# Kernel tuning notes

Measured on AMD Instinct MI355X. Metric: run time of the kernel, lower is better.

The kernel has to match this reference:

```python
import jax, jax.numpy as jnp
import numpy as np

N = 4096  # matrix is [N, N]; all entries are nonzero 'edges' (uniform(0,1) fill)


def setup_inputs() -> dict:
    key = jax.random.key(0)
    k1, k2, k3 = jax.random.split(key, 3)
    matrix = jax.random.uniform(k1, (N, N), dtype=jnp.float32)
    drop_param = jax.random.normal(k2, (1,), dtype=jnp.float32)
    gamma = jax.random.normal(k3, (1,), dtype=jnp.float32)
    return {"matrix": matrix, "drop_param": drop_param, "gamma": gamma,
            "drop_ratio_pct": 20}


def reference(matrix, drop_param, gamma, drop_ratio_pct):
    # Flatten: every nonzero entry is an edge. With uniform fill all N*N entries
    # are edges, so num_edges is static and k is a trace-time Python int.
    v = matrix.reshape(-1)                       # [E] edge values
    num_edges = v.shape[0]
    k = (num_edges * drop_ratio_pct) // 100      # int(num_edges * drop_ratio)

    # drop_prob = sigmoid(drop_param*(1 - v) - gamma*v)  (per-edge weight)
    logits = drop_param[0] * (1.0 - v) - gamma[0] * v
    logp = jax.nn.log_sigmoid(logits)            # log of unnormalized weight

    # Weighted sampling without replacement (Efraimidis-Spirakis / Gumbel top-k):
    # taking top-k of log(p_i) + Gumbel_i samples k indices w/o replacement with
    # probability proportional to p_i (normalization is a shift, top-k invariant).
    u = jax.random.uniform(jax.random.key(42), (num_edges,), dtype=jnp.float32,
                           minval=1e-7, maxval=1.0 - 1e-7)
    gumbel = -jnp.log(-jnp.log(u))
    keys = jnp.where(v != 0, logp + gumbel, -jnp.inf)  # only real edges eligible
    _, drop_idx = jax.lax.top_k(keys, k)         # [k] sampled edge indices

    # Vectorized scatter of zeros (replaces the Python for-loop in the original)
    dropped = v.at[drop_idx].set(0.0)
    return dropped.reshape(matrix.shape)
```

## Files before the change

### kernel.cpp

```cpp
#include <hip/hip_runtime.h>
#include <hip/hip_bf16.h>
#include <stdint.h>


#define NBINS 8192
#define NBINS_SHIFT 19
#define NB 512
#define NB2 256
#define LIST_CAP 1572864u
#define MINI_CAP 16384u
#define DELTA 1e-3f
#define LBUF_CAP 2048
#define TIES_TILE 4096

__device__ __forceinline__ unsigned tf_bits(unsigned i) {
  const unsigned ks0 = 0u;
  const unsigned ks1 = 42u;
  const unsigned ks2 = 0x1BD11BDAu ^ 0u ^ 42u;
  unsigned x0 = 0u + ks0;
  unsigned x1 = i + ks1;
#define TF_R(rot) { x0 += x1; x1 = (x1 << (rot)) | (x1 >> (32 - (rot))); x1 ^= x0; }
  TF_R(13) TF_R(15) TF_R(26) TF_R(6)
  x0 += ks1; x1 += ks2 + 1u;
  TF_R(17) TF_R(29) TF_R(16) TF_R(24)
  x0 += ks2; x1 += ks0 + 2u;
  TF_R(13) TF_R(15) TF_R(26) TF_R(6)
  x0 += ks0; x1 += ks1 + 3u;
  TF_R(17) TF_R(29) TF_R(16) TF_R(24)
  x0 += ks1; x1 += ks2 + 4u;
  TF_R(13) TF_R(15) TF_R(26) TF_R(6)
  x0 += ks2; x1 += ks0 + 5u;
#undef TF_R
  return x0 ^ x1;
}

__device__ __forceinline__ float uniform_from_bits(unsigned bits) {
  unsigned fb = (bits >> 9) | 0x3f800000u;
  float f = __uint_as_float(fb) - 1.0f;
  const float minv = 1e-7f;
  const float maxv = __uint_as_float(0x3F7FFFFEu);
  float r = __fsub_rn(maxv, minv);
  float u = __fadd_rn(__fmul_rn(f, r), minv);
  return fmaxf(minv, u);
}

__device__ __forceinline__ float xla_expf(float input) {
  const float exp_hi = 88.3762626647950f;
  const float exp_lo = -88.3762626647949f;
  float x = fminf(fmaxf(input, exp_lo), exp_hi);
  float fx = floorf(__fadd_rn(__fmul_rn(x, 1.44269504088896341f), 0.5f));
  float tmp = __fmul_rn(0.693359375f, fx);
  float z = __fmul_rn(-2.12194440e-4f, fx);
  x = __fsub_rn(x, tmp);
  x = __fsub_rn(x, z);
  z = __fmul_rn(x, x);
  float y = __fadd_rn(__fmul_rn(x, 1.9875691500e-4f), 1.3981999507e-3f);
  y = __fadd_rn(__fmul_rn(y, x), 8.3334519073e-3f);
  y = __fadd_rn(__fmul_rn(y, x), 4.1665795894e-2f);
  y = __fadd_rn(__fmul_rn(y, x), 1.6666665459e-1f);
  y = __fadd_rn(__fmul_rn(y, x), 5.0000001201e-1f);
  y = __fadd_rn(__fmul_rn(y, z), x);
  y = __fadd_rn(1.0f, y);
  int n = (int)fx;
  float p2n = __int_as_float((n + 0x7f) << 23);
  return fmaxf(__fmul_rn(y, p2n), input);
}

__device__ __forceinline__ float xla_logf(float input) {
  float t0 = fmaxf(input, __uint_as_float(0x00800000u));
  unsigned ib = __float_as_uint(t0);
  int emm0 = (int)(ib >> 23) - 0x7f;
  float e = __fadd_rn(1.0f, (float)emm0);
  float m = __uint_as_float((ib & 0x807fffffu) | 0x3f000000u);
  bool mask = m < 0.707106781186547524f;
  float t1 = mask ? m : 0.0f;
  m = __fsub_rn(m, 1.0f);
  e = __fsub_rn(e, mask ? 1.0f : 0.0f);
  m = __fadd_rn(m, t1);
  float x2 = __fmul_rn(m, m);
  float x3 = __fmul_rn(x2, m);
  float y  = __fadd_rn(__fmul_rn(m, 7.0376836292e-2f), -1.1514610310e-1f);
  float y1 = __fadd_rn(__fmul_rn(m, -1.2420140846e-1f), 1.4249322787e-1f);
  float y2 = __fadd_rn(__fmul_rn(m, 2.0000714765e-1f), -2.4999993993e-1f);
  y  = __fadd_rn(__fmul_rn(y, m), 1.1676998740e-1f);
  y1 = __fadd_rn(__fmul_rn(y1, m), -1.6668057665e-1f);
  y2 = __fadd_rn(__fmul_rn(y2, m), 3.3333331174e-1f);
  y = __fadd_rn(__fmul_rn(y, x3), y1);
  y = __fadd_rn(__fmul_rn(y, x3), y2);
  y = __fmul_rn(y, x3);
  y = __fadd_rn(y, __fmul_rn(-2.12194440e-4f, e));
  y = __fsub_rn(y, __fmul_rn(0.5f, x2));
  m = __fadd_rn(m, y);
  m = __fadd_rn(m, __fmul_rn(0.693359375f, e));
  return m;
}

__device__ __forceinline__ float xla_log1pf(float x) {
  float for_large = xla_logf(__fadd_rn(x, 1.0f));
  float for_small = __fmul_rn(__fadd_rn(__fmul_rn(-0.5f, x), 1.0f), x);
  return (fabsf(x) < 1e-4f) ? for_small : for_large;
}

__device__ __forceinline__ unsigned encode_f(float f) {
  unsigned b = __float_as_uint(f);
  return (b & 0x80000000u) ? ~b : (b | 0x80000000u);
}
__device__ __forceinline__ float decode_f(unsigned c) {
  unsigned b = (c & 0x80000000u) ? (c ^ 0x80000000u) : ~c;
  return __uint_as_float(b);
}

__device__ __forceinline__ unsigned compute_ou(unsigned i, float v, float dp, float g) {
  if (v == 0.0f) return 0u;
  unsigned bits = tf_bits(i);
  float u = uniform_from_bits(bits);
  float lg = xla_logf(u);
  float gum = -xla_logf(-lg);
  float t = __fsub_rn(1.0f, v);
  float lx = __fsub_rn(__fmul_rn(dp, t), __fmul_rn(g, v));
  float ex = xla_expf(-fabsf(lx));
  float l1p = xla_log1pf(ex);
  float lp = -(__fadd_rn(fmaxf(-lx, 0.0f), l1p));
  float key = __fadd_rn(lp, gum);
  return encode_f(key);
}

__device__ __forceinline__ unsigned approx_code(unsigned i, float v, float dp, float g) {
  if (v == 0.0f) return 0u;
  unsigned bits = tf_bits(i);
  float u = uniform_from_bits(bits);
  float lg = __logf(u);
  float gum = -__logf(-lg);
  float t = __fsub_rn(1.0f, v);
  float lx = __fsub_rn(__fmul_rn(dp, t), __fmul_rn(g, v));
  float ex = __expf(-fabsf(lx));
  float for_small = __fmul_rn(__fadd_rn(__fmul_rn(-0.5f, ex), 1.0f), ex);
  float l1p = (fabsf(ex) < 1e-4f) ? for_small : __logf(__fadd_rn(ex, 1.0f));
  float lp = -(__fadd_rn(fmaxf(-lx, 0.0f), l1p));
  float key = __fadd_rn(lp, gum);
  return encode_f(key);
}

__global__ __launch_bounds__(512) void key_hist1_kernel(
    const float* __restrict__ v, const float* __restrict__ dpp,
    const float* __restrict__ gp, unsigned* __restrict__ keys,
    unsigned* __restrict__ blockhist, int E) {
  __shared__ unsigned h[NBINS];
  for (int j = threadIdx.x; j < NBINS; j += 512) h[j] = 0;
  __syncthreads();
  float dp = dpp[0], g = gp[0];
  int nvec = E >> 2;
  int stride = gridDim.x * 512;
  for (int iv = blockIdx.x * 512 + threadIdx.x; iv < nvec; iv += stride) {
    float4 vv = reinterpret_cast<const float4*>(v)[iv];
    unsigned base = (unsigned)iv << 2;
    unsigned o0, o1, o2, o3;
    if (keys) {
      o0 = approx_code(base + 0u, vv.x, dp, g);
      o1 = approx_code(base + 1u, vv.y, dp, g);
      o2 = approx_code(base + 2u, vv.z, dp, g);
      o3 = approx_code(base + 3u, vv.w, dp, g);
      reinterpret_cast<uint4*>(keys)[iv] = make_uint4(o0, o1, o2, o3);
    } else {
      o0 = compute_ou(base + 0u, vv.x, dp, g);
      o1 = compute_ou(base + 1u, vv.y, dp, g);
      o2 = compute_ou(base + 2u, vv.z, dp, g);
      o3 = compute_ou(base + 3u, vv.w, dp, g);
    }
    atomicAdd(&h[o0 >> NBINS_SHIFT], 1u);
    atomicAdd(&h[o1 >> NBINS_SHIFT], 1u);
    atomicAdd(&h[o2 >> NBINS_SHIFT], 1u);
    atomicAdd(&h[o3 >> NBINS_SHIFT], 1u);
  }
  if (blockIdx.x == 0) {
    for (int i = (nvec << 2) + threadIdx.x; i < E; i += 512) {
      float val = v[i];
      unsigned ou = keys ? approx_code((unsigned)i, val, dp, g)
                         : compute_ou((unsigned)i, val, dp, g);
      if (keys) keys[i] = ou;
      atomicAdd(&h[ou >> NBINS_SHIFT], 1u);
    }
  }
  __syncthreads();
  unsigned* row = blockhist + (size_t)blockIdx.x * NBINS;
  for (int j = threadIdx.x; j < NBINS; j += 512) row[j] = h[j];
}

#define RED_SLICES 8
__global__ __launch_bounds__(256) void reduce_hist_kernel(
    const unsigned* __restrict__ blockhist, unsigned* __restrict__ hist) {
  int gid = blockIdx.x * 256 + threadIdx.x;
  int j = gid & (NBINS - 1);
  int slice = gid >> 13;
  unsigned s = 0;
  for (int b = slice; b < NB; b += RED_SLICES)
    s += blockhist[(size_t)b * NBINS + j];
  atomicAdd(&hist[j], s);
}

__global__ __launch_bounds__(1024) void find_sel_kernel(
    const unsigned* __restrict__ hist, unsigned* __restrict__ state,
    const int* __restrict__ pct_p, long long Etot, float delta) {
  __shared__ unsigned s[1024];
  int t = threadIdx.x;
  unsigned hh[8];
  unsigned tot = 0;
  #pragma unroll
  for (int j = 0; j < 8; ++j) { hh[j] = hist[t * 8 + j]; tot += hh[j]; }
  s[t] = tot;
  __syncthreads();
  for (int off = 1; off < 1024; off <<= 1) {
    unsigned add = (t + off < 1024) ? s[t + off] : 0u;
    __syncthreads();
    s[t] += add;
    __syncthreads();
  }
  long long k = (Etot * (long long)pct_p[0]) / 100;
  long long above_next = (t < 1023) ? (long long)s[t + 1] : 0;
  if (above_next < k && k <= above_next + (long long)tot) {
    long long above = above_next;
    int b = 7;
    for (; b >= 0; --b) {
      if (above < k && k <= above + (long long)hh[b]) break;
      above += (long long)hh[b];
    }
    unsigned B = (unsigned)(t * 8 + b);
    state[0] = B;
    state[6] = (unsigned)k;
    float L = decode_f(B << NBINS_SHIFT);
    unsigned blo = encode_f(L - delta);
    unsigned bhi;
    if (B == NBINS - 1u) bhi = 0xFFFFFFFFu;
    else {
      float H = decode_f((B + 1u) << NBINS_SHIFT);
      bhi = encode_f(H + delta);
    }
    state[2] = blo;
    state[3] = bhi;
    unsigned span = bhi - blo;
    unsigned sh = 0;
    while ((span >> sh) >= 4096u) ++sh;
    state[12] = sh;
  }
}

__global__ __launch_bounds__(512) void output_kernel(
    const float* __restrict__ v, const float* __restrict__ dpp,
    const float* __restrict__ gp, const unsigned* __restrict__ keys,
    float* __restrict__ out, unsigned* __restrict__ state,
    unsigned* __restrict__ list, int E) {
  __shared__ unsigned lcnt, lbase, sacc;
  __shared__ unsigned lbuf[LBUF_CAP];
  if (threadIdx.x == 0) { lcnt = 0; sacc = 0; }
  __syncthreads();
  unsigned blo = state[2], bhi = state[3];
  float dp = dpp[0], g = gp[0];
  int nvec = E >> 2;
  int stride = gridDim.x * 512;
  unsigned acnt = 0;
  for (int iv = blockIdx.x * 512 + threadIdx.x; iv < nvec; iv += stride) {
    float4 vv = reinterpret_cast<const float4*>(v)[iv];
    unsigned base = (unsigned)iv << 2;
    unsigned os[4];
    if (keys) {
      uint4 kk = reinterpret_cast<const uint4*>(keys)[iv];
      os[0] = kk.x; os[1] = kk.y; os[2] = kk.z; os[3] = kk.w;
    } else {
      os[0] = compute_ou(base + 0u, vv.x, dp, g);
      os[1] = compute_ou(base + 1u, vv.y, dp, g);
      os[2] = compute_ou(base + 2u, vv.z, dp, g);
      os[3] = compute_ou(base + 3u, vv.w, dp, g);
    }
    float vals[4] = {vv.x, vv.y, vv.z, vv.w};
    float4 oo;
    float res[4];
    #pragma unroll
    for (int j = 0; j < 4; ++j) {
      bool drop = os[j] > bhi;
      acnt += drop ? 1u : 0u;
      res[j] = drop ? 0.0f : vals[j];
      if (!drop && os[j] >= blo) {
        unsigned p = atomicAdd(&lcnt, 1u);
        if (p < LBUF_CAP) lbuf[p] = base + (unsigned)j;
        else {
          unsigned q = atomicAdd(&state[4], 1u);
          if (q < LIST_CAP) list[q] = base + (unsigned)j;
        }
      }
    }
    oo.x = res[0]; oo.y = res[1]; oo.z = res[2]; oo.w = res[3];
    reinterpret_cast<float4*>(out)[iv] = oo;
  }
  if (blockIdx.x == 0) {
    for (int i = (nvec << 2) + threadIdx.x; i < E; i += 512) {
      float val = v[i];
      unsigned ou = keys ? keys[i] : compute_ou((unsigned)i, val, dp, g);
      bool drop = ou > bhi;
      acnt += drop ? 1u : 0u;
      out[i] = drop ? 0.0f : val;
      if (!drop && ou >= blo) {
        unsigned p = atomicAdd(&lcnt, 1u);
        if (p < LBUF_CAP) lbuf[p] = (unsigned)i;
        else {
          unsigned q = atomicAdd(&state[4], 1u);
          if (q < LIST_CAP) list[q] = (unsigned)i;
        }
      }
    }
  }
  #pragma unroll
  for (int off = 32; off > 0; off >>= 1) acnt += __shfl_xor(acnt, off);
  if ((threadIdx.x & 63) == 0 && acnt) atomicAdd(&sacc, acnt);
  __syncthreads();
  if (threadIdx.x == 0) {
    unsigned n = min(lcnt, (unsigned)LBUF_CAP);
    lbase = atomicAdd(&state[4], n);
    if (sacc) atomicAdd(&state[5], sacc);
  }
  __syncthreads();
  unsigned n = min(lcnt, (unsigned)LBUF_CAP);
  for (unsigned j = threadIdx.x; j < n; j += 512) {
    unsigned q = lbase + j;
    if (q < LIST_CAP) list[q] = lbuf[j];
  }
}

__device__ __forceinline__ unsigned band_bin(unsigned ec, unsigned blo,
                                             unsigned span, unsigned sh) {
  if (ec <= blo) return 0u;
  unsigned d = ec - blo;
  if (d > span) d = span;
  return d >> sh;
}

__global__ __launch_bounds__(256) void exact_eval_kernel(
    const float* __restrict__ v, const float* __restrict__ dpp,
    const float* __restrict__ gp, const unsigned* __restrict__ list,
    unsigned* __restrict__ elist, const unsigned* __restrict__ state,
    unsigned* __restrict__ blockhist2) {
  __shared__ unsigned h[4096];
  for (int j = threadIdx.x; j < 4096; j += 256) h[j] = 0;
  __syncthreads();
  unsigned M = min(state[4], LIST_CAP);
  unsigned blo = state[2], span = state[3] - state[2], sh = state[12];
  float dp = dpp[0], g = gp[0];
  for (unsigned e = blockIdx.x * 256 + threadIdx.x; e < M; e += gridDim.x * 256) {
    unsigned idx = list[e];
    unsigned ec = compute_ou(idx, v[idx], dp, g);
    elist[e] = ec;
    atomicAdd(&h[band_bin(ec, blo, span, sh)], 1u);
  }
  __syncthreads();
  unsigned* row = blockhist2 + (size_t)blockIdx.x * 4096;
  for (int j = threadIdx.x; j < 4096; j += 256) row[j] = h[j];
}

__global__ __launch_bounds__(256) void reduce_hist2_kernel(
    const unsigned* __restrict__ blockhist2, unsigned* __restrict__ hist2) {
  int j = blockIdx.x * 256 + threadIdx.x;
  unsigned s = 0;
  for (int b = 0; b < NB2; ++b) s += blockhist2[(size_t)b * 4096 + j];
  hist2[j] = s;
}

__global__ __launch_bounds__(1024) void find_band_kernel(
    const unsigned* __restrict__ hist2, unsigned* __restrict__ state) {
  __shared__ unsigned s[1024];
  int t = threadIdx.x;
  unsigned hh[4];
  unsigned tot = 0;
  #pragma unroll
  for (int j = 0; j < 4; ++j) { hh[j] = hist2[t * 4 + j]; tot += hh[j]; }
  s[t] = tot;
  __syncthreads();
  for (int off = 1; off < 1024; off <<= 1) {
    unsigned add = (t + off < 1024) ? s[t + off] : 0u;
    __syncthreads();
    s[t] += add;
    __syncthreads();
  }
  unsigned kp = state[6] - state[5];
  if (kp == 0u || kp > s[0]) {
    if (t == 0) { state[7] = 0xFFFFFFFFu; state[8] = 0u; }
    return;
  }
  unsigned above_next = (t < 1023) ? s[t + 1] : 0u;
  if (above_next < kp && kp <= s[t]) {
    unsigned above = above_next;
    for (int b = 3; b >= 0; --b) {
      if (above < kp && kp <= above + hh[b]) {
        state[7] = (unsigned)(t * 4 + b);
        state[8] = kp - above;
        break;
      }
      above += hh[b];
    }
  }
}

__global__ __launch_bounds__(256) void band_drop_kernel(
    const unsigned* __restrict__ list, const unsigned* __restrict__ elist,
    unsigned* __restrict__ state, float* __restrict__ out,
    uint2* __restrict__ mini) {
  unsigned M = min(state[4], LIST_CAP);
  unsigned Eb = state[7];
  unsigned blo = state[2], span = state[3] - state[2], sh = state[12];
  for (unsigned e = blockIdx.x * 256 + threadIdx.x; e < M; e += gridDim.x * 256) {
    unsigned ec = elist[e];
    unsigned bin = band_bin(ec, blo, span, sh);
    if (bin > Eb) out[list[e]] = 0.0f;
    else if (bin == Eb) {
      unsigned q = atomicAdd(&state[11], 1u);
      if (q < MINI_CAP) mini[q] = make_uint2(ec, list[e]);
    }
  }
}

__global__ __launch_bounds__(1024) void mini_ties_kernel(
    const uint2* __restrict__ mini, const unsigned* __restrict__ state,
    float* __restrict__ out) {
  __shared__ uint2 tile[TIES_TILE];
  unsigned m = min(state[11], MINI_CAP);
  unsigned r = state[8];
  if (r == 0u || m == 0u) return;
  int tid = threadIdx.x;
  for (unsigned e0 = 0; e0 < m; e0 += blockDim.x) {
    unsigned e = e0 + tid;
    bool valid = e < m;
    unsigned my_ec = 0, my_idx = 0;
    if (valid) { uint2 me = mini[e]; my_ec = me.x; my_idx = me.y; }
    unsigned rank = 0;
    for (unsigned t0 = 0; t0 < m; t0 += TIES_TILE) {
      unsigned tn = min((unsigned)TIES_TILE, m - t0);
      __syncthreads();
      for (unsigned j = tid; j < tn; j += blockDim.x) tile[j] = mini[t0 + j];
      __syncthreads();
      if (valid) {
        for (unsigned j = 0; j < tn; ++j) {
          uint2 o = tile[j];
          rank += (o.x > my_ec || (o.x == my_ec && o.y < my_idx)) ? 1u : 0u;
        }
      }
    }
    if (valid && rank < r) out[my_idx] = 0.0f;
  }
}

extern "C" void kernel_launch(void* const* d_in, const int* in_sizes, int n_in,
                              void* d_out, int out_size, void* d_ws, size_t ws_size,
                              hipStream_t stream) {
  const float* v  = (const float*)d_in[0];
  const float* dp = (const float*)d_in[1];
  const float* g  = (const float*)d_in[2];
  const int* pct  = (const int*)d_in[3];
  float* out = (float*)d_out;
  int E = in_sizes[0];

  uint8_t* ws = (uint8_t*)d_ws;
  const size_t STATE_OFF = 0;
  const size_t HIST_OFF  = 4096;
  const size_t HIST2_OFF = 40 * 1024;
  const size_t MINI_OFF  = 64 * 1024;
  const size_t BH_OFF    = (size_t)1 << 20;
  const size_t BH2_OFF   = (size_t)1 << 20;
  const size_t LIST_OFF  = (size_t)5 << 20;
  const size_t ELIST_OFF = (size_t)11 << 20;
  const size_t KEYS_OFF  = (size_t)17 << 20;

  if (ws_size < BH_OFF + (size_t)NB * NBINS * 4) {
    hipMemcpyAsync(out, v, (size_t)E * 4, hipMemcpyDeviceToDevice, stream);
    return;
  }
  bool use_keys = ws_size >= KEYS_OFF + (size_t)E * 4;

  unsigned* state  = (unsigned*)(ws + STATE_OFF);
  unsigned* hist   = (unsigned*)(ws + HIST_OFF);
  unsigned* hist2  = (unsigned*)(ws + HIST2_OFF);
  uint2*    mini   = (uint2*)(ws + MINI_OFF);
  unsigned* bh     = (unsigned*)(ws + BH_OFF);
  unsigned* bh2    = (unsigned*)(ws + BH2_OFF);
  unsigned* list   = (unsigned*)(ws + LIST_OFF);
  unsigned* elist  = (unsigned*)(ws + ELIST_OFF);
  unsigned* keys   = use_keys ? (unsigned*)(ws + KEYS_OFF) : nullptr;
  float delta = use_keys ? DELTA : 0.0f;

  hipMemsetAsync(ws, 0, (size_t)1 << 20, stream);

  key_hist1_kernel<<<NB, 512, 0, stream>>>(v, dp, g, keys, bh, E);
  reduce_hist_kernel<<<256, 256, 0, stream>>>(bh, hist);
  find_sel_kernel<<<1, 1024, 0, stream>>>(hist, state, pct, (long long)E, delta);
  output_kernel<<<1024, 512, 0, stream>>>(v, dp, g, keys, out, state, list, E);
  exact_eval_kernel<<<NB2, 256, 0, stream>>>(v, dp, g, list, elist, state, bh2);
  reduce_hist2_kernel<<<16, 256, 0, stream>>>(bh2, hist2);
  find_band_kernel<<<1, 1024, 0, stream>>>(hist2, state);
  band_drop_kernel<<<256, 256, 0, stream>>>(list, elist, state, out, mini);
  mini_ties_kernel<<<1, 1024, 0, stream>>>(mini, state, out);
}
```

Baseline: 155.0 us.

## Estimate threshold bin from sample, fuse key/hist/output pass with verify fallback

Replaces the full-pass key materialization plus separate output pass with a sampled histogram that guesses the threshold bin, followed by one fused pass that computes keys, builds the full histogram, writes the output and collects candidates in a ±SLACK bin window. A verify kernel checks whether the true threshold bin lies strictly inside the window and, if not, triggers a second full pass with a tight window. Candidate list entries now carry the value so the exact evaluation no longer gathers from the matrix. This removes the keys buffer write and reread, at the cost of a possibly wider candidate band and a rare extra full pass.

After: 422.9 us. +172.8%, slower.

```diff
diff --git a/kernel.cpp b/kernel.cpp
--- a/kernel.cpp
+++ b/kernel.cpp
@@ -6,12 +6,13 @@
 #define NBINS 8192
 #define NBINS_SHIFT 19
 #define NB 512
+#define NBS 64
 #define NB2 256
 #define LIST_CAP 1572864u
 #define MINI_CAP 16384u
-#define DELTA 1e-3f
 #define LBUF_CAP 2048
 #define TIES_TILE 4096
+#define SLACK 8
 
 __device__ __forceinline__ unsigned tf_bits(unsigned i) {
   const unsigned ks0 = 0u;
@@ -105,10 +106,6 @@
   unsigned b = __float_as_uint(f);
   return (b & 0x80000000u) ? ~b : (b | 0x80000000u);
 }
-__device__ __forceinline__ float decode_f(unsigned c) {
-  unsigned b = (c & 0x80000000u) ? (c ^ 0x80000000u) : ~c;
-  return __uint_as_float(b);
-}
 
 __device__ __forceinline__ unsigned compute_ou(unsigned i, float v, float dp, float g) {
   if (v == 0.0f) return 0u;
@@ -141,49 +138,163 @@
   return encode_f(key);
 }
 
-__global__ __launch_bounds__(512) void key_hist1_kernel(
+__global__ __launch_bounds__(1024) void sample_hist_kernel(
     const float* __restrict__ v, const float* __restrict__ dpp,
-    const float* __restrict__ gp, unsigned* __restrict__ keys,
-    unsigned* __restrict__ blockhist, int E) {
+    const float* __restrict__ gp, unsigned* __restrict__ hist_s,
+    int nvec, int chunk, int spb) {
   __shared__ unsigned h[NBINS];
-  for (int j = threadIdx.x; j < NBINS; j += 512) h[j] = 0;
-  __syncthreads();
+  for (int j = threadIdx.x; j < NBINS; j += 1024) h[j] = 0;
+  __syncthreads();
+  float dp = dpp[0], g = gp[0];
+  int t = threadIdx.x;
+  if (t < spb) {
+    int iv = blockIdx.x * chunk + t;
+    if (iv < nvec) {
+      float4 vv = reinterpret_cast<const float4*>(v)[iv];
+      unsigned base = (unsigned)iv << 2;
+      atomicAdd(&h[approx_code(base + 0u, vv.x, dp, g) >> NBINS_SHIFT], 1u);
+      atomicAdd(&h[approx_code(base + 1u, vv.y, dp, g) >> NBINS_SHIFT], 1u);
+      atomicAdd(&h[approx_code(base + 2u, vv.z, dp, g) >> NBINS_SHIFT], 1u);
+      atomicAdd(&h[approx_code(base + 3u, vv.w, dp, g) >> NBINS_SHIFT], 1u);
+    }
+  }
+  __syncthreads();
+  for (int j = threadIdx.x; j < NBINS; j += 1024)
+    if (h[j]) atomicAdd(&hist_s[j], h[j]);
+}
+
+__global__ __launch_bounds__(1024) void find_sample_kernel(
+    const unsigned* __restrict__ hist_s, unsigned* __restrict__ state,
+    const int* __restrict__ pct_p, long long Etot, long long SN) {
+  __shared__ unsigned s[1024];
+  __shared__ int bs_sh;
+  int t = threadIdx.x;
+  if (t == 0) bs_sh = 0;
+  unsigned hh[8];
+  unsigned tot = 0;
+  #pragma unroll
+  for (int j = 0; j < 8; ++j) { hh[j] = hist_s[t * 8 + j]; tot += hh[j]; }
+  s[t] = tot;
+  __syncthreads();
+  for (int off = 1; off < 1024; off <<= 1) {
+    unsigned add = (t + off < 1024) ? s[t + off] : 0u;
+    __syncthreads();
+    s[t] += add;
+    __syncthreads();
+  }
+  long long k = (Etot * (long long)pct_p[0]) / 100;
+  long long ks = (SN > 0 && Etot > 0) ? (k * SN) / Etot : 0;
+  if (ks < 1) ks = 1;
+  long long above_next = (t < 1023) ? (long long)s[t + 1] : 0;
+  if (above_next < ks && ks <= above_next + (long long)tot) {
+    long long above = above_next;
+    for (int b = 7; b >= 0; --b) {
+      if (above < ks && ks <= above + (long long)hh[b]) { bs_sh = t * 8 + b; break; }
+      above += (long long)hh[b];
+    }
+  }
+  __syncthreads();
+  if (t == 0) {
+    state[6] = (unsigned)k;
+    int B = bs_sh;
+    int plo = B - SLACK; if (plo < 0) plo = 0;
+    int phi = B + SLACK; if (phi > NBINS - 1) phi = NBINS - 1;
+    state[13] = (unsigned)plo;
+    state[14] = (unsigned)phi;
+    unsigned blo = (unsigned)plo << NBINS_SHIFT;
+    unsigned bhi = (phi == NBINS - 1) ? 0xFFFFFFFFu
+                                      : ((((unsigned)phi + 1u) << NBINS_SHIFT) - 1u);
+    if (k == 0) { blo = 0xFFFFFFFFu; bhi = 0xFFFFFFFFu; }
+    state[2] = blo;
+    state[3] = bhi;
+  }
+}
+
+__global__ __launch_bounds__(1024) void stream_kernel(
+    const float* __restrict__ v, const float* __restrict__ dpp,
+    const float* __restrict__ gp, float* __restrict__ out,
+    unsigned* __restrict__ state, uint2* __restrict__ list,
+    unsigned* __restrict__ blockhist, int E, int mode) {
+  if (mode == 1 && state[15] == 0u) return;
+  __shared__ unsigned h[NBINS];
+  __shared__ uint2 lbuf[LBUF_CAP];
+  __shared__ unsigned lcnt, lbase, sacc;
+  if (threadIdx.x == 0) { lcnt = 0; sacc = 0; }
+  if (mode == 0) for (int j = threadIdx.x; j < NBINS; j += 1024) h[j] = 0;
+  __syncthreads();
+  unsigned blo = state[2], bhi = state[3];
   float dp = dpp[0], g = gp[0];
   int nvec = E >> 2;
-  int stride = gridDim.x * 512;
-  for (int iv = blockIdx.x * 512 + threadIdx.x; iv < nvec; iv += stride) {
+  int stride = gridDim.x * 1024;
+  unsigned acnt = 0;
+  for (int iv = blockIdx.x * 1024 + threadIdx.x; iv < nvec; iv += stride) {
     float4 vv = reinterpret_cast<const float4*>(v)[iv];
     unsigned base = (unsigned)iv << 2;
-    unsigned o0, o1, o2, o3;
-    if (keys) {
-      o0 = approx_code(base + 0u, vv.x, dp, g);
-      o1 = approx_code(base + 1u, vv.y, dp, g);
-      o2 = approx_code(base + 2u, vv.z, dp, g);
-      o3 = approx_code(base + 3u, vv.w, dp, g);
-      reinterpret_cast<uint4*>(keys)[iv] = make_uint4(o0, o1, o2, o3);
-    } else {
-      o0 = compute_ou(base + 0u, vv.x, dp, g);
-      o1 = compute_ou(base + 1u, vv.y, dp, g);
-      o2 = compute_ou(base + 2u, vv.z, dp, g);
-      o3 = compute_ou(base + 3u, vv.w, dp, g);
-    }
-    atomicAdd(&h[o0 >> NBINS_SHIFT], 1u);
-    atomicAdd(&h[o1 >> NBINS_SHIFT], 1u);
-    atomicAdd(&h[o2 >> NBINS_SHIFT], 1u);
-    atomicAdd(&h[o3 >> NBINS_SHIFT], 1u);
+    float vals[4] = {vv.x, vv.y, vv.z, vv.w};
+    unsigned os[4];
+    #pragma unroll
+    for (int j = 0; j < 4; ++j) os[j] = approx_code(base + (unsigned)j, vals[j], dp, g);
+    if (mode == 0) {
+      #pragma unroll
+      for (int j = 0; j < 4; ++j) atomicAdd(&h[os[j] >> NBINS_SHIFT], 1u);
+    }
+    float res[4];
+    #pragma unroll
+    for (int j = 0; j < 4; ++j) {
+      bool drop = os[j] > bhi;
+      acnt += drop ? 1u : 0u;
+      res[j] = drop ? 0.0f : vals[j];
+      if (!drop && os[j] >= blo) {
+        unsigned p = atomicAdd(&lcnt, 1u);
+        uint2 ent = make_uint2(base + (unsigned)j, __float_as_uint(vals[j]));
+        if (p < LBUF_CAP) lbuf[p] = ent;
+        else {
+          unsigned q = atomicAdd(&state[4], 1u);
+          if (q < LIST_CAP) list[q] = ent;
+        }
+      }
+    }
+    float4 oo; oo.x = res[0]; oo.y = res[1]; oo.z = res[2]; oo.w = res[3];
+    reinterpret_cast<float4*>(out)[iv] = oo;
   }
   if (blockIdx.x == 0) {
-    for (int i = (nvec << 2) + threadIdx.x; i < E; i += 512) {
+    for (int i = (nvec << 2) + threadIdx.x; i < E; i += 1024) {
       float val = v[i];
-      unsigned ou = keys ? approx_code((unsigned)i, val, dp, g)
-                         : compute_ou((unsigned)i, val, dp, g);
-      if (keys) keys[i] = ou;
-      atomicAdd(&h[ou >> NBINS_SHIFT], 1u);
-    }
-  }
-  __syncthreads();
-  unsigned* row = blockhist + (size_t)blockIdx.x * NBINS;
-  for (int j = threadIdx.x; j < NBINS; j += 512) row[j] = h[j];
+      unsigned ou = approx_code((unsigned)i, val, dp, g);
+      if (mode == 0) atomicAdd(&h[ou >> NBINS_SHIFT], 1u);
+      bool drop = ou > bhi;
+      acnt += drop ? 1u : 0u;
+      out[i] = drop ? 0.0f : val;
+      if (!drop && ou >= blo) {
+        unsigned p = atomicAdd(&lcnt, 1u);
+        uint2 ent = make_uint2((unsigned)i, __float_as_uint(val));
+        if (p < LBUF_CAP) lbuf[p] = ent;
+        else {
+          unsigned q = atomicAdd(&state[4], 1u);
+          if (q < LIST_CAP) list[q] = ent;
+        }
+      }
+    }
+  }
+  #pragma unroll
+  for (int off = 32; off > 0; off >>= 1) acnt += __shfl_xor(acnt, off);
+  if ((threadIdx.x & 63) == 0 && acnt) atomicAdd(&sacc, acnt);
+  __syncthreads();
+  if (threadIdx.x == 0) {
+    unsigned n = min(lcnt, (unsigned)LBUF_CAP);
+    lbase = atomicAdd(&state[4], n);
+    if (sacc) atomicAdd(&state[5], sacc);
+  }
+  __syncthreads();
+  if (mode == 0) {
+    unsigned* row = blockhist + (size_t)blockIdx.x * NBINS;
+    for (int j = threadIdx.x; j < NBINS; j += 1024) row[j] = h[j];
+  }
+  unsigned n = min(lcnt, (unsigned)LBUF_CAP);
+  for (unsigned j = threadIdx.x; j < n; j += 1024) {
+    unsigned q = lbase + j;
+    if (q < LIST_CAP) list[q] = lbuf[j];
+  }
 }
 
 #define RED_SLICES 8
@@ -198,11 +309,12 @@
   atomicAdd(&hist[j], s);
 }
 
-__global__ __launch_bounds__(1024) void find_sel_kernel(
-    const unsigned* __restrict__ hist, unsigned* __restrict__ state,
-    const int* __restrict__ pct_p, long long Etot, float delta) {
+__global__ __launch_bounds__(1024) void find_verify_kernel(
+    const unsigned* __restrict__ hist, unsigned* __restrict__ state) {
   __shared__ unsigned s[1024];
+  __shared__ int bstar_sh;
   int t = threadIdx.x;
+  if (t == 0) bstar_sh = 0;
   unsigned hh[8];
   unsigned tot = 0;
   #pragma unroll
@@ -215,113 +327,43 @@
     s[t] += add;
     __syncthreads();
   }
-  long long k = (Etot * (long long)pct_p[0]) / 100;
-  long long above_next = (t < 1023) ? (long long)s[t + 1] : 0;
-  if (above_next < k && k <= above_next + (long long)tot) {
-    long long above = above_next;
-    int b = 7;
-    for (; b >= 0; --b) {
-      if (above < k && k <= above + (long long)hh[b]) break;
-      above += (long long)hh[b];
-    }
-    unsigned B = (unsigned)(t * 8 + b);
-    state[0] = B;
-    state[6] = (unsigned)k;
-    float L = decode_f(B << NBINS_SHIFT);
-    unsigned blo = encode_f(L - delta);
-    unsigned bhi;
-    if (B == NBINS - 1u) bhi = 0xFFFFFFFFu;
-    else {
-      float H = decode_f((B + 1u) << NBINS_SHIFT);
-      bhi = encode_f(H + delta);
-    }
-    state[2] = blo;
-    state[3] = bhi;
-    unsigned span = bhi - blo;
-    unsigned sh = 0;
-    while ((span >> sh) >= 4096u) ++sh;
-    state[12] = sh;
-  }
-}
-
-__global__ __launch_bounds__(512) void output_kernel(
-    const float* __restrict__ v, const float* __restrict__ dpp,
-    const float* __restrict__ gp, const unsigned* __restrict__ keys,
-    float* __restrict__ out, unsigned* __restrict__ state,
-    unsigned* __restrict__ list, int E) {
-  __shared__ unsigned lcnt, lbase, sacc;
-  __shared__ unsigned lbuf[LBUF_CAP];
-  if (threadIdx.x == 0) { lcnt = 0; sacc = 0; }
-  __syncthreads();
-  unsigned blo = state[2], bhi = state[3];
-  float dp = dpp[0], g = gp[0];
-  int nvec = E >> 2;
-  int stride = gridDim.x * 512;
-  unsigned acnt = 0;
-  for (int iv = blockIdx.x * 512 + threadIdx.x; iv < nvec; iv += stride) {
-    float4 vv = reinterpret_cast<const float4*>(v)[iv];
-    unsigned base = (unsigned)iv << 2;
-    unsigned os[4];
-    if (keys) {
-      uint4 kk = reinterpret_cast<const uint4*>(keys)[iv];
-      os[0] = kk.x; os[1] = kk.y; os[2] = kk.z; os[3] = kk.w;
+  unsigned k = state[6];
+  if (k > 0u) {
+    unsigned above_next = (t < 1023) ? s[t + 1] : 0u;
+    if (above_next < k && k <= s[t]) {
+      unsigned above = above_next;
+      for (int b = 7; b >= 0; --b) {
+        if (above < k && k <= above + hh[b]) { bstar_sh = t * 8 + b; break; }
+        above += hh[b];
+      }
+    }
+  }
+  __syncthreads();
+  if (t == 0) {
+    if (k == 0u) {
+      state[15] = 0u;
+      state[12] = 0u;
     } else {
-      os[0] = compute_ou(base + 0u, vv.x, dp, g);
-      os[1] = compute_ou(base + 1u, vv.y, dp, g);
-      os[2] = compute_ou(base + 2u, vv.z, dp, g);
-      os[3] = compute_ou(base + 3u, vv.w, dp, g);
-    }
-    float vals[4] = {vv.x, vv.y, vv.z, vv.w};
-    float4 oo;
-    float res[4];
-    #pragma unroll
-    for (int j = 0; j < 4; ++j) {
-      bool drop = os[j] > bhi;
-      acnt += drop ? 1u : 0u;
-      res[j] = drop ? 0.0f : vals[j];
-      if (!drop && os[j] >= blo) {
-        unsigned p = atomicAdd(&lcnt, 1u);
-        if (p < LBUF_CAP) lbuf[p] = base + (unsigned)j;
-        else {
-          unsigned q = atomicAdd(&state[4], 1u);
-          if (q < LIST_CAP) list[q] = base + (unsigned)j;
-        }
+      int Bs = bstar_sh;
+      int plo = (int)state[13], phi = (int)state[14];
+      bool ok = (Bs >= plo + 1) && (Bs <= phi - 1) && (state[4] <= LIST_CAP);
+      if (ok) {
+        state[15] = 0u;
+      } else {
+        state[15] = 1u;
+        int p2lo = (Bs > 0) ? Bs - 1 : 0;
+        int p2hi = (Bs < NBINS - 1) ? Bs + 1 : NBINS - 1;
+        state[2] = (unsigned)p2lo << NBINS_SHIFT;
+        state[3] = (p2hi == NBINS - 1) ? 0xFFFFFFFFu
+                                       : ((((unsigned)p2hi + 1u) << NBINS_SHIFT) - 1u);
+        state[4] = 0u;
+        state[5] = 0u;
       }
-    }
-    oo.x = res[0]; oo.y = res[1]; oo.z = res[2]; oo.w = res[3];
-    reinterpret_cast<float4*>(out)[iv] = oo;
-  }
-  if (blockIdx.x == 0) {
-    for (int i = (nvec << 2) + threadIdx.x; i < E; i += 512) {
-      float val = v[i];
-      unsigned ou = keys ? keys[i] : compute_ou((unsigned)i, val, dp, g);
-      bool drop = ou > bhi;
-      acnt += drop ? 1u : 0u;
-      out[i] = drop ? 0.0f : val;
-      if (!drop && ou >= blo) {
-        unsigned p = atomicAdd(&lcnt, 1u);
-        if (p < LBUF_CAP) lbuf[p] = (unsigned)i;
-        else {
-          unsigned q = atomicAdd(&state[4], 1u);
-          if (q < LIST_CAP) list[q] = (unsigned)i;
-        }
-      }
-    }
-  }
-  #pragma unroll
-  for (int off = 32; off > 0; off >>= 1) acnt += __shfl_xor(acnt, off);
-  if ((threadIdx.x & 63) == 0 && acnt) atomicAdd(&sacc, acnt);
-  __syncthreads();
-  if (threadIdx.x == 0) {
-    unsigned n = min(lcnt, (unsigned)LBUF_CAP);
-    lbase = atomicAdd(&state[4], n);
-    if (sacc) atomicAdd(&state[5], sacc);
-  }
-  __syncthreads();
-  unsigned n = min(lcnt, (unsigned)LBUF_CAP);
-  for (unsigned j = threadIdx.x; j < n; j += 512) {
-    unsigned q = lbase + j;
-    if (q < LIST_CAP) list[q] = lbuf[j];
+      unsigned span = state[3] - state[2];
+      unsigned sh = 0;
+      while ((span >> sh) >= 4096u) ++sh;
+      state[12] = sh;
+    }
   }
 }
 
@@ -334,10 +376,9 @@
 }
 
 __global__ __launch_bounds__(256) void exact_eval_kernel(
-    const float* __restrict__ v, const float* __restrict__ dpp,
-    const float* __restrict__ gp, const unsigned* __restrict__ list,
-    unsigned* __restrict__ elist, const unsigned* __restrict__ state,
-    unsigned* __restrict__ blockhist2) {
+    const float* __restrict__ dpp, const float* __restrict__ gp,
+    const uint2* __restrict__ list, unsigned* __restrict__ elist,
+    const unsigned* __restrict__ state, unsigned* __restrict__ blockhist2) {
   __shared__ unsigned h[4096];
   for (int j = threadIdx.x; j < 4096; j += 256) h[j] = 0;
   __syncthreads();
@@ -345,8 +386,8 @@
   unsigned blo = state[2], span = state[3] - state[2], sh = state[12];
   float dp = dpp[0], g = gp[0];
   for (unsigned e = blockIdx.x * 256 + threadIdx.x; e < M; e += gridDim.x * 256) {
-    unsigned idx = list[e];
-    unsigned ec = compute_ou(idx, v[idx], dp, g);
+    uint2 le = list[e];
+    unsigned ec = compute_ou(le.x, __uint_as_float(le.y), dp, g);
     elist[e] = ec;
     atomicAdd(&h[band_bin(ec, blo, span, sh)], 1u);
   }
@@ -399,7 +440,7 @@
 }
 
 __global__ __launch_bounds__(256) void band_drop_kernel(
-    const unsigned* __restrict__ list, const unsigned* __restrict__ elist,
+    const uint2* __restrict__ list, const unsigned* __restrict__ elist,
     unsigned* __restrict__ state, float* __restrict__ out,
     uint2* __restrict__ mini) {
   unsigned M = min(state[4], LIST_CAP);
@@ -408,10 +449,10 @@
   for (unsigned e = blockIdx.x * 256 + threadIdx.x; e < M; e += gridDim.x * 256) {
     unsigned ec = elist[e];
     unsigned bin = band_bin(ec, blo, span, sh);
-    if (bin > Eb) out[list[e]] = 0.0f;
+    if (bin > Eb) out[list[e].x] = 0.0f;
     else if (bin == Eb) {
       unsigned q = atomicAdd(&state[11], 1u);
-      if (q < MINI_CAP) mini[q] = make_uint2(ec, list[e]);
+      if (q < MINI_CAP) mini[q] = make_uint2(ec, list[e].x);
     }
   }
 }
@@ -458,39 +499,45 @@
 
   uint8_t* ws = (uint8_t*)d_ws;
   const size_t STATE_OFF = 0;
-  const size_t HIST_OFF  = 4096;
-  const size_t HIST2_OFF = 40 * 1024;
-  const size_t MINI_OFF  = 64 * 1024;
+  const size_t HIST_OFF  = 4 * 1024;
+  const size_t HISTS_OFF = 36 * 1024;
+  const size_t HIST2_OFF = 68 * 1024;
+  const size_t MINI_OFF  = 128 * 1024;
   const size_t BH_OFF    = (size_t)1 << 20;
   const size_t BH2_OFF   = (size_t)1 << 20;
-  const size_t LIST_OFF  = (size_t)5 << 20;
-  const size_t ELIST_OFF = (size_t)11 << 20;
-  const size_t KEYS_OFF  = (size_t)17 << 20;
-
-  if (ws_size < BH_OFF + (size_t)NB * NBINS * 4) {
+  const size_t LIST_OFF  = (size_t)17 << 20;
+  const size_t ELIST_OFF = (size_t)29 << 20;
+  const size_t NEED = ELIST_OFF + (size_t)LIST_CAP * 4;
+
+  if (ws_size < NEED) {
     hipMemcpyAsync(out, v, (size_t)E * 4, hipMemcpyDeviceToDevice, stream);
     return;
   }
-  bool use_keys = ws_size >= KEYS_OFF + (size_t)E * 4;
 
   unsigned* state  = (unsigned*)(ws + STATE_OFF);
   unsigned* hist   = (unsigned*)(ws + HIST_OFF);
+  unsigned* hist_s = (unsigned*)(ws + HISTS_OFF);
   unsigned* hist2  = (unsigned*)(ws + HIST2_OFF);
   uint2*    mini   = (uint2*)(ws + MINI_OFF);
   unsigned* bh     = (unsigned*)(ws + BH_OFF);
   unsigned* bh2    = (unsigned*)(ws + BH2_OFF);
-  unsigned* list   = (unsigned*)(ws + LIST_OFF);
+  uint2*    list   = (uint2*)(ws + LIST_OFF);
   unsigned* elist  = (unsigned*)(ws + ELIST_OFF);
-  unsigned* keys   = use_keys ? (unsigned*)(ws + KEYS_OFF) : nullptr;
-  float delta = use_keys ? DELTA : 0.0f;
+
+  int nvec = E >> 2;
+  int chunk = nvec / NBS;
+  int spb = chunk < 1024 ? chunk : 1024;
+  long long SN = (long long)NBS * (long long)spb * 4;
 
   hipMemsetAsync(ws, 0, (size_t)1 << 20, stream);
 
-  key_hist1_kernel<<<NB, 512, 0, stream>>>(v, dp, g, keys, bh, E);
+  sample_hist_kernel<<<NBS, 1024, 0, stream>>>(v, dp, g, hist_s, nvec, chunk, spb);
+  find_sample_kernel<<<1, 1024, 0, stream>>>(hist_s, state, pct, (long long)E, SN);
+  stream_kernel<<<NB, 1024, 0, stream>>>(v, dp, g, out, state, list, bh, E, 0);
   reduce_hist_kernel<<<256, 256, 0, stream>>>(bh, hist);
-  find_sel_kernel<<<1, 1024, 0, stream>>>(hist, state, pct, (long long)E, delta);
-  output_kernel<<<1024, 512, 0, stream>>>(v, dp, g, keys, out, state, list, E);
-  exact_eval_kernel<<<NB2, 256, 0, stream>>>(v, dp, g, list, elist, state, bh2);
+  find_verify_kernel<<<1, 1024, 0, stream>>>(hist, state);
+  stream_kernel<<<NB, 1024, 0, stream>>>(v, dp, g, out, state, list, bh, E, 1);
+  exact_eval_kernel<<<NB2, 256, 0, stream>>>(dp, g, list, elist, state, bh2);
   reduce_hist2_kernel<<<16, 256, 0, stream>>>(bh2, hist2);
   find_band_kernel<<<1, 1024, 0, stream>>>(hist2, state);
   band_drop_kernel<<<256, 256, 0, stream>>>(list, elist, state, out, mini);
```
